# Kernel tuning notes

Hardware: AMD Instinct MI355X
Metric: run time of the kernel (lower is better)

Reference implementation:

```python
import jax, jax.numpy as jnp
import numpy as np

D = 256          # num_channels
H = 4            # num_heads
DH = D // H      # head dim
BN_EPS = 1e-5


def conv1x1(x, W, b):
    # x: [B, Cin, N], W: [Cout, Cin], b: [Cout] -> [B, Cout, N]
    return jnp.einsum('oc,bcn->bon', W, x) + b[None, :, None]


def bn_eval(x, gamma, beta):
    # eval-mode BatchNorm1d with running_mean=0, running_var=1
    scale = gamma / jnp.sqrt(1.0 + BN_EPS)
    return x * scale[None, :, None] + beta[None, :, None]


def setup_inputs() -> dict:
    key = jax.random.key(0)
    ks = jax.random.split(key, 16)
    B, N = 1, 4096
    s = 0.05
    inp = {
        'corr_feat_belief': jax.random.normal(ks[0], (B, D, N), dtype=jnp.float32),
        'spatial_compatibility': jax.random.uniform(ks[1], (B, N, N), dtype=jnp.float32),
        'Wq': jax.random.normal(ks[2], (D, D), dtype=jnp.float32) * s,
        'bq': jnp.zeros((D,), jnp.float32),
        'Wk': jax.random.normal(ks[3], (D, D), dtype=jnp.float32) * s,
        'bk': jnp.zeros((D,), jnp.float32),
        'Wv': jax.random.normal(ks[4], (D, D), dtype=jnp.float32) * s,
        'bv': jnp.zeros((D,), jnp.float32),
        'W1': jax.random.normal(ks[5], (D // 2, D), dtype=jnp.float32) * s,
        'b1': jnp.zeros((D // 2,), jnp.float32),
        'g1': jnp.ones((D // 2,), jnp.float32),
        'be1': jnp.zeros((D // 2,), jnp.float32),
        'W2': jax.random.normal(ks[6], (D // 2, D // 2), dtype=jnp.float32) * s,
        'b2': jnp.zeros((D // 2,), jnp.float32),
        'g2': jnp.ones((D // 2,), jnp.float32),
        'be2': jnp.zeros((D // 2,), jnp.float32),
        'W3': jax.random.normal(ks[7], (D, D // 2), dtype=jnp.float32) * s,
        'b3': jnp.zeros((D,), jnp.float32),
    }
    return inp


def reference(corr_feat_belief, spatial_compatibility, Wq, bq, Wk, bk, Wv, bv,
              W1, b1, g1, be1, W2, b2, g2, be2, W3, b3):
    x = corr_feat_belief                      # [B, D, N]
    B, _, N = x.shape
    # QKV conv1x1 projections, split heads -> [B, H, DH, N]
    Q = conv1x1(x, Wq, bq).reshape(B, H, DH, N)
    K = conv1x1(x, Wk, bk).reshape(B, H, DH, N)
    V = conv1x1(x, Wv, bv).reshape(B, H, DH, N)
    # attention scores [B, H, N, N], scaled
    att = jnp.einsum('bhco,bhci->bhoi', Q, K) / np.sqrt(DH).astype(np.float32)
    # multiplicative spatial-compatibility mask, softmax over keys
    weight = jax.nn.softmax(spatial_compatibility[:, None, :, :] * att, axis=-1)
    message = jnp.einsum('bhoi,bhci->bhco', weight, V).reshape(B, D, N)
    # message MLP: conv1x1 -> BN -> ReLU -> conv1x1 -> BN -> ReLU -> conv1x1
    h = jax.nn.relu(bn_eval(conv1x1(message, W1, b1), g1, be1))
    h = jax.nn.relu(bn_eval(conv1x1(h, W2, b2), g2, be2))
    h = conv1x1(h, W3, b3)
    return x + h
```

## Files before the change

kernel.cpp:

```cpp
#include <hip/hip_runtime.h>
#include <hip/hip_bf16.h>
#include <math.h>

#define D_CH   256
#define NHEAD  4
#define DHEAD  64
#define NPTS   4096
#define KSPLIT 8
#define KCHUNK (NPTS / KSPLIT)
#define BN_RSQ 0.99999500003749963f
#define HSTRIDE 262144

typedef __attribute__((ext_vector_type(4))) float f32x4;
typedef __attribute__((ext_vector_type(8))) short bf16x8;
typedef unsigned short ushort_t;

__device__ __forceinline__ ushort_t f2bf(float x) {
    unsigned int b = __float_as_uint(x);
    return (ushort_t)((b + 0x7FFF + ((b >> 16) & 1)) >> 16);
}
__device__ __forceinline__ float bf2f(ushort_t u) {
    return __uint_as_float(((unsigned int)u) << 16);
}
__device__ __forceinline__ unsigned cvt_pk(float lo, float hi) {
    unsigned r;
    asm("v_cvt_pk_bf16_f32 %0, %1, %2" : "=v"(r) : "v"(lo), "v"(hi));
    return r;
}

__global__ __launch_bounds__(256) void transpose_cast(
    const float* __restrict__ x, ushort_t* __restrict__ xT)
{
    __shared__ float xs[64][65];
    const int tid = threadIdx.x;
    const int n0 = blockIdx.x * 64, k0 = blockIdx.y * 64;
#pragma unroll
    for (int p = 0; p < 16; ++p) {
        int kk = p * 4 + (tid >> 6), nn = tid & 63;
        xs[kk][nn] = x[(size_t)(k0 + kk) * NPTS + n0 + nn];
    }
    __syncthreads();
#pragma unroll
    for (int p = 0; p < 16; ++p) {
        int nn = p * 4 + (tid >> 6), kk = tid & 63;
        xT[(size_t)(n0 + nn) * D_CH + k0 + kk] = f2bf(xs[kk][nn]);
    }
}

__device__ __forceinline__ void gemm_tile_body(
    const float* __restrict__ A, const ushort_t* __restrict__ Bt,
    int K, int m0, int n0, int l15, int lhi, f32x4 acc[2][2])
{
#pragma unroll
    for (int i = 0; i < 2; ++i)
#pragma unroll
        for (int j = 0; j < 2; ++j) acc[i][j] = (f32x4){0.f, 0.f, 0.f, 0.f};

    for (int k0 = 0; k0 < K; k0 += 32) {
        bf16x8 af[2], bfr[2];
#pragma unroll
        for (int mf = 0; mf < 2; ++mf) {
            const float* ap = A + (size_t)(m0 + mf * 16 + l15) * K + k0 + lhi * 8;
            float4 a0 = *(const float4*)ap;
            float4 a1 = *(const float4*)(ap + 4);
            unsigned* tp = (unsigned*)&af[mf];
            tp[0] = cvt_pk(a0.x, a0.y);
            tp[1] = cvt_pk(a0.z, a0.w);
            tp[2] = cvt_pk(a1.x, a1.y);
            tp[3] = cvt_pk(a1.z, a1.w);
        }
#pragma unroll
        for (int nf = 0; nf < 2; ++nf)
            bfr[nf] = *(const bf16x8*)&Bt[(size_t)(n0 + nf * 16 + l15) * K + k0 + lhi * 8];
#pragma unroll
        for (int mf = 0; mf < 2; ++mf)
#pragma unroll
            for (int nf = 0; nf < 2; ++nf)
                acc[mf][nf] = __builtin_amdgcn_mfma_f32_16x16x32_bf16(af[mf], bfr[nf], acc[mf][nf], 0, 0, 0);
    }
}

__global__ __launch_bounds__(256) void gemm_qkv(
    const float* __restrict__ Wq, const float* __restrict__ bq,
    const float* __restrict__ Wk, const float* __restrict__ bk,
    const float* __restrict__ Wv, const float* __restrict__ bv,
    const ushort_t* __restrict__ xT,
    ushort_t* __restrict__ Qf, ushort_t* __restrict__ Kf, ushort_t* __restrict__ Vf)
{
    const int tid = threadIdx.x;
    const int w = tid >> 6, lane = tid & 63, l15 = lane & 15, lhi = lane >> 4;
    const int wm = w >> 1, wn = w & 1;
    const int m0 = blockIdx.y * 64 + wm * 32;
    const int n0 = blockIdx.x * 64 + wn * 32;
    const int z = blockIdx.z;

    const float* A    = (z == 0) ? Wq : (z == 1) ? Wk : Wv;
    const float* bias = (z == 0) ? bq : (z == 1) ? bk : bv;
    ushort_t* dst     = (z == 0) ? Qf : (z == 1) ? Kf : Vf;
    const float scl   = (z == 0) ? 0.125f : 1.0f;

    f32x4 acc[2][2];
    gemm_tile_body(A, xT, D_CH, m0, n0, l15, lhi, acc);

#pragma unroll
    for (int mf = 0; mf < 2; ++mf) {
#pragma unroll
        for (int r = 0; r < 4; ++r) {
            int m = m0 + mf * 16 + lhi * 4 + r;
            int head = m >> 6, dch = m & 63;
            float bi = bias[m];
#pragma unroll
            for (int nf = 0; nf < 2; ++nf) {
                int n = n0 + nf * 16 + l15;
                float v = (acc[mf][nf][r] + bi) * scl;
                size_t idx;
                if (z < 2)
                    idx = (size_t)head * HSTRIDE + (size_t)(n >> 4) * 1024 + (dch >> 5) * 512
                        + (((dch >> 3) & 3) * 16 + (n & 15)) * 8 + (dch & 7);
                else
                    idx = (size_t)head * HSTRIDE + (size_t)(n >> 6) * 4096 + (dch >> 4) * 1024
                        + ((n >> 5) & 1) * 512 + (((n >> 3) & 3) * 16 + (dch & 15)) * 8 + (n & 7);
                dst[idx] = (ushort_t)(cvt_pk(v, v) & 0xFFFF);
            }
        }
    }
}

__device__ __forceinline__ void attn_tile(
    int kt, int ktn, const float* __restrict__ Sg,
    const ushort_t* __restrict__ Kh, const ushort_t* __restrict__ Vh,
    const bf16x8 (&qf)[2][2],
    ushort_t (* __restrict__ Sw)[72],
    f32x4 (&macc)[2][4], float (&lrun)[2],
    ushort_t (* __restrict__ Pw)[72], int l15, int lhi, int lane)
{
    f32x4 sr[8];
#pragma unroll
    for (int p = 0; p < 8; ++p)
        sr[p] = *(const f32x4*)&Sg[(size_t)p * 4 * NPTS + (size_t)ktn * 64];

    bf16x8 vf[8];
    const ushort_t* vb = Vh + (size_t)kt * 4096 + lane * 8;
#pragma unroll
    for (int mm = 0; mm < 2; ++mm)
#pragma unroll
        for (int db = 0; db < 4; ++db)
            vf[mm * 4 + db] = *(const bf16x8*)(vb + db * 1024 + mm * 512);

    f32x4 sacc0[4], sacc1[4];
    __builtin_amdgcn_s_setprio(1);
#pragma unroll
    for (int kb = 0; kb < 4; ++kb) {
        const ushort_t* kp = Kh + (size_t)(kt * 4 + kb) * 1024 + lane * 8;
        bf16x8 kf0 = *(const bf16x8*)kp;
        bf16x8 kf1 = *(const bf16x8*)(kp + 512);
        f32x4 z0 = (f32x4){0.f, 0.f, 0.f, 0.f};
        z0 = __builtin_amdgcn_mfma_f32_16x16x32_bf16(kf0, qf[0][0], z0, 0, 0, 0);
        z0 = __builtin_amdgcn_mfma_f32_16x16x32_bf16(kf1, qf[0][1], z0, 0, 0, 0);
        sacc0[kb] = z0;
        f32x4 z1 = (f32x4){0.f, 0.f, 0.f, 0.f};
        z1 = __builtin_amdgcn_mfma_f32_16x16x32_bf16(kf0, qf[1][0], z1, 0, 0, 0);
        z1 = __builtin_amdgcn_mfma_f32_16x16x32_bf16(kf1, qf[1][1], z1, 0, 0, 0);
        sacc1[kb] = z1;
    }
    __builtin_amdgcn_s_setprio(0);

    float ts0 = 0.0f, ts1 = 0.0f;
#pragma unroll
    for (int kb = 0; kb < 4; ++kb) {
        unsigned a0 = *(const unsigned*)&Sw[l15][kb * 16 + lhi * 4];
        unsigned a1 = *(const unsigned*)&Sw[l15][kb * 16 + lhi * 4 + 2];
        unsigned b0 = *(const unsigned*)&Sw[16 + l15][kb * 16 + lhi * 4];
        unsigned b1 = *(const unsigned*)&Sw[16 + l15][kb * 16 + lhi * 4 + 2];
        float p00 = __expf(sacc0[kb][0] * bf2f((ushort_t)(a0 & 0xFFFF)));
        float p01 = __expf(sacc0[kb][1] * bf2f((ushort_t)(a0 >> 16)));
        float p02 = __expf(sacc0[kb][2] * bf2f((ushort_t)(a1 & 0xFFFF)));
        float p03 = __expf(sacc0[kb][3] * bf2f((ushort_t)(a1 >> 16)));
        float p10 = __expf(sacc1[kb][0] * bf2f((ushort_t)(b0 & 0xFFFF)));
        float p11 = __expf(sacc1[kb][1] * bf2f((ushort_t)(b0 >> 16)));
        float p12 = __expf(sacc1[kb][2] * bf2f((ushort_t)(b1 & 0xFFFF)));
        float p13 = __expf(sacc1[kb][3] * bf2f((ushort_t)(b1 >> 16)));
        ts0 += (p00 + p01) + (p02 + p03);
        ts1 += (p10 + p11) + (p12 + p13);
        *(unsigned*)&Pw[l15][kb * 16 + lhi * 4]          = cvt_pk(p00, p01);
        *(unsigned*)&Pw[l15][kb * 16 + lhi * 4 + 2]      = cvt_pk(p02, p03);
        *(unsigned*)&Pw[16 + l15][kb * 16 + lhi * 4]     = cvt_pk(p10, p11);
        *(unsigned*)&Pw[16 + l15][kb * 16 + lhi * 4 + 2] = cvt_pk(p12, p13);
    }
    lrun[0] += ts0;
    lrun[1] += ts1;

    __builtin_amdgcn_s_setprio(1);
#pragma unroll
    for (int mm = 0; mm < 2; ++mm) {
        bf16x8 pf0 = *(const bf16x8*)&Pw[l15][mm * 32 + lhi * 8];
        bf16x8 pf1 = *(const bf16x8*)&Pw[16 + l15][mm * 32 + lhi * 8];
#pragma unroll
        for (int db = 0; db < 4; ++db) {
            macc[0][db] = __builtin_amdgcn_mfma_f32_16x16x32_bf16(vf[mm * 4 + db], pf0, macc[0][db], 0, 0, 0);
            macc[1][db] = __builtin_amdgcn_mfma_f32_16x16x32_bf16(vf[mm * 4 + db], pf1, macc[1][db], 0, 0, 0);
        }
    }
    __builtin_amdgcn_s_setprio(0);

#pragma unroll
    for (int p = 0; p < 8; ++p) {
        *(unsigned*)&Sw[p * 4 + lhi][l15 * 4]     = cvt_pk(sr[p][0], sr[p][1]);
        *(unsigned*)&Sw[p * 4 + lhi][l15 * 4 + 2] = cvt_pk(sr[p][2], sr[p][3]);
    }
}

__global__ __launch_bounds__(256, 3) void attn_mfma(
    const ushort_t* __restrict__ Qf, const ushort_t* __restrict__ Kf,
    const ushort_t* __restrict__ Vf, const float* __restrict__ S,
    ushort_t* __restrict__ pacc, float* __restrict__ pl)
{
    __shared__ __align__(16) ushort_t P_lds[4][32][72];
    __shared__ __align__(16) ushort_t S_lds[4][32][72];

    const int tid  = threadIdx.x;
    const int w    = tid >> 6;
    const int lane = tid & 63;
    const int l15  = lane & 15;
    const int lhi  = lane >> 4;
    const int h    = blockIdx.y;
    const int ks   = blockIdx.z;
    const int q0   = blockIdx.x * 128 + w * 32;
    const int ktb  = ks * (KCHUNK / 64);

    const ushort_t* Kh = Kf + (size_t)h * HSTRIDE;
    const ushort_t* Vh = Vf + (size_t)h * HSTRIDE;
    const float* Sg = S + (size_t)(q0 + lhi) * NPTS + l15 * 4;
    ushort_t (* __restrict__ Pw)[72] = P_lds[w];
    ushort_t (* __restrict__ Sw)[72] = S_lds[w];

    bf16x8 qf[2][2];
#pragma unroll
    for (int f = 0; f < 2; ++f) {
        const ushort_t* qp = Qf + (size_t)h * HSTRIDE
                           + (size_t)((q0 + f * 16) >> 4) * 1024 + lane * 8;
        qf[f][0] = *(const bf16x8*)qp;
        qf[f][1] = *(const bf16x8*)(qp + 512);
    }

    f32x4 macc[2][4];
#pragma unroll
    for (int f = 0; f < 2; ++f)
#pragma unroll
        for (int db = 0; db < 4; ++db) macc[f][db] = (f32x4){0.f, 0.f, 0.f, 0.f};
    float lrun[2] = {0.0f, 0.0f};

    {
#pragma unroll
        for (int p = 0; p < 8; ++p) {
            f32x4 t = *(const f32x4*)&Sg[(size_t)p * 4 * NPTS + (size_t)ktb * 64];
            *(unsigned*)&Sw[p * 4 + lhi][l15 * 4]     = cvt_pk(t[0], t[1]);
            *(unsigned*)&Sw[p * 4 + lhi][l15 * 4 + 2] = cvt_pk(t[2], t[3]);
        }
    }

    for (int kt = ktb; kt < ktb + 8; ++kt) {
        const int ktn = (kt + 1 < ktb + 8) ? kt + 1 : ktb;
        attn_tile(kt, ktn, Sg, Kh, Vh, qf, Sw, macc, lrun, Pw, l15, lhi, lane);
    }

#pragma unroll
    for (int f = 0; f < 2; ++f) {
        lrun[f] += __shfl_xor(lrun[f], 16);
        lrun[f] += __shfl_xor(lrun[f], 32);
    }

    const size_t pb = ((size_t)ks * NHEAD + h) * NPTS;
#pragma unroll
    for (int f = 0; f < 2; ++f) {
        ushort_t* prow = pacc + (pb + q0 + f * 16 + l15) * DHEAD;
#pragma unroll
        for (int db = 0; db < 4; ++db) {
            *(unsigned*)&prow[db * 16 + lhi * 4]     = cvt_pk(macc[f][db][0], macc[f][db][1]);
            *(unsigned*)&prow[db * 16 + lhi * 4 + 2] = cvt_pk(macc[f][db][2], macc[f][db][3]);
        }
    }
    if (lane < 16) {
        pl[pb + q0 + lane]      = lrun[0];
        pl[pb + q0 + 16 + lane] = lrun[1];
    }
}

__global__ __launch_bounds__(256) void mlp_fused(
    const ushort_t* __restrict__ pacc, const float* __restrict__ pl,
    ushort_t* __restrict__ msgT,
    const float* __restrict__ W1, const float* __restrict__ b1,
    const float* __restrict__ g1, const float* __restrict__ be1,
    const float* __restrict__ W2, const float* __restrict__ b2,
    const float* __restrict__ g2, const float* __restrict__ be2,
    const float* __restrict__ W3, const float* __restrict__ b3,
    const float* __restrict__ x, float* __restrict__ out,
    ushort_t* __restrict__ h1T, ushort_t* __restrict__ h2T)
{
    const int tid = threadIdx.x;
    const int w = tid >> 6, lane = tid & 63, l15 = lane & 15, lhi = lane >> 4;
    const int nblk = blockIdx.x * 16;

    {
        const int hb  = (tid >> 7) * 2;
        const int loc = tid & 127;
        const int ql  = loc >> 3;
        const int d0  = (loc & 7) * 8;
#pragma unroll
        for (int hh = 0; hh < 2; ++hh) {
            const int h = hb + hh;
            float ls = 0.0f;
#pragma unroll
            for (int ks = 0; ks < KSPLIT; ++ks)
                ls += pl[((size_t)ks * NHEAD + h) * NPTS + nblk + ql];
            float inv = 1.0f / ls;
            float o[8];
#pragma unroll
            for (int j = 0; j < 8; ++j) o[j] = 0.0f;
#pragma unroll
            for (int ks = 0; ks < KSPLIT; ++ks) {
                const ushort_t* ap = pacc
                    + (((size_t)ks * NHEAD + h) * NPTS + nblk + ql) * DHEAD + d0;
                bf16x8 v = *(const bf16x8*)ap;
#pragma unroll
                for (int j = 0; j < 8; ++j) o[j] += bf2f((ushort_t)v[j]);
            }
            unsigned* dp = (unsigned*)(msgT + (size_t)(nblk + ql) * D_CH + h * 64 + d0);
            dp[0] = cvt_pk(o[0] * inv, o[1] * inv);
            dp[1] = cvt_pk(o[2] * inv, o[3] * inv);
            dp[2] = cvt_pk(o[4] * inv, o[5] * inv);
            dp[3] = cvt_pk(o[6] * inv, o[7] * inv);
        }
    }
    __syncthreads();

    {
        f32x4 acc[2];
        acc[0] = (f32x4){0.f, 0.f, 0.f, 0.f};
        acc[1] = (f32x4){0.f, 0.f, 0.f, 0.f};
        const ushort_t* Bt = msgT + (size_t)nblk * D_CH;
        for (int k0 = 0; k0 < 256; k0 += 32) {
            bf16x8 bfr = *(const bf16x8*)&Bt[(size_t)l15 * D_CH + k0 + lhi * 8];
#pragma unroll
            for (int mf = 0; mf < 2; ++mf) {
                const float* ap = W1 + (size_t)(w * 32 + mf * 16 + l15) * 256 + k0 + lhi * 8;
                float4 a0 = *(const float4*)ap;
                float4 a1 = *(const float4*)(ap + 4);
                bf16x8 af;
                unsigned* tp = (unsigned*)&af;
                tp[0] = cvt_pk(a0.x, a0.y); tp[1] = cvt_pk(a0.z, a0.w);
                tp[2] = cvt_pk(a1.x, a1.y); tp[3] = cvt_pk(a1.z, a1.w);
                acc[mf] = __builtin_amdgcn_mfma_f32_16x16x32_bf16(af, bfr, acc[mf], 0, 0, 0);
            }
        }
#pragma unroll
        for (int mf = 0; mf < 2; ++mf)
#pragma unroll
            for (int r = 0; r < 4; ++r) {
                int m = w * 32 + mf * 16 + lhi * 4 + r;
                float bi = b1[m], sc = g1[m] * BN_RSQ, sh = be1[m];
                float v = fmaxf((acc[mf][r] + bi) * sc + sh, 0.0f);
                h1T[(size_t)(nblk + l15) * 128 + m] = (ushort_t)(cvt_pk(v, v) & 0xFFFF);
            }
    }
    __syncthreads();

    {
        f32x4 acc[2];
        acc[0] = (f32x4){0.f, 0.f, 0.f, 0.f};
        acc[1] = (f32x4){0.f, 0.f, 0.f, 0.f};
        const ushort_t* Bt = h1T + (size_t)nblk * 128;
        for (int k0 = 0; k0 < 128; k0 += 32) {
            bf16x8 bfr = *(const bf16x8*)&Bt[(size_t)l15 * 128 + k0 + lhi * 8];
#pragma unroll
            for (int mf = 0; mf < 2; ++mf) {
                const float* ap = W2 + (size_t)(w * 32 + mf * 16 + l15) * 128 + k0 + lhi * 8;
                float4 a0 = *(const float4*)ap;
                float4 a1 = *(const float4*)(ap + 4);
                bf16x8 af;
                unsigned* tp = (unsigned*)&af;
                tp[0] = cvt_pk(a0.x, a0.y); tp[1] = cvt_pk(a0.z, a0.w);
                tp[2] = cvt_pk(a1.x, a1.y); tp[3] = cvt_pk(a1.z, a1.w);
                acc[mf] = __builtin_amdgcn_mfma_f32_16x16x32_bf16(af, bfr, acc[mf], 0, 0, 0);
            }
        }
#pragma unroll
        for (int mf = 0; mf < 2; ++mf)
#pragma unroll
            for (int r = 0; r < 4; ++r) {
                int m = w * 32 + mf * 16 + lhi * 4 + r;
                float bi = b2[m], sc = g2[m] * BN_RSQ, sh = be2[m];
                float v = fmaxf((acc[mf][r] + bi) * sc + sh, 0.0f);
                h2T[(size_t)(nblk + l15) * 128 + m] = (ushort_t)(cvt_pk(v, v) & 0xFFFF);
            }
    }
    __syncthreads();

    {
        f32x4 acc[4];
#pragma unroll
        for (int i = 0; i < 4; ++i) acc[i] = (f32x4){0.f, 0.f, 0.f, 0.f};
        const ushort_t* Bt = h2T + (size_t)nblk * 128;
        for (int k0 = 0; k0 < 128; k0 += 32) {
            bf16x8 bfr = *(const bf16x8*)&Bt[(size_t)l15 * 128 + k0 + lhi * 8];
#pragma unroll
            for (int mf = 0; mf < 4; ++mf) {
                const float* ap = W3 + (size_t)(w * 64 + mf * 16 + l15) * 128 + k0 + lhi * 8;
                float4 a0 = *(const float4*)ap;
                float4 a1 = *(const float4*)(ap + 4);
                bf16x8 af;
                unsigned* tp = (unsigned*)&af;
                tp[0] = cvt_pk(a0.x, a0.y); tp[1] = cvt_pk(a0.z, a0.w);
                tp[2] = cvt_pk(a1.x, a1.y); tp[3] = cvt_pk(a1.z, a1.w);
                acc[mf] = __builtin_amdgcn_mfma_f32_16x16x32_bf16(af, bfr, acc[mf], 0, 0, 0);
            }
        }
#pragma unroll
        for (int mf = 0; mf < 4; ++mf)
#pragma unroll
            for (int r = 0; r < 4; ++r) {
                int m = w * 64 + mf * 16 + lhi * 4 + r;
                float bi = b3[m];
                int n = nblk + l15;
                out[(size_t)m * NPTS + n] = acc[mf][r] + bi + x[(size_t)m * NPTS + n];
            }
    }
}

extern "C" void kernel_launch(void* const* d_in, const int* in_sizes, int n_in,
                              void* d_out, int out_size, void* d_ws, size_t ws_size,
                              hipStream_t stream) {
    const float* x  = (const float*)d_in[0];
    const float* S  = (const float*)d_in[1];
    const float* Wq = (const float*)d_in[2];
    const float* bq = (const float*)d_in[3];
    const float* Wk = (const float*)d_in[4];
    const float* bk = (const float*)d_in[5];
    const float* Wv = (const float*)d_in[6];
    const float* bv = (const float*)d_in[7];
    const float* W1 = (const float*)d_in[8];
    const float* b1 = (const float*)d_in[9];
    const float* g1 = (const float*)d_in[10];
    const float* be1= (const float*)d_in[11];
    const float* W2 = (const float*)d_in[12];
    const float* b2 = (const float*)d_in[13];
    const float* g2 = (const float*)d_in[14];
    const float* be2= (const float*)d_in[15];
    const float* W3 = (const float*)d_in[16];
    const float* b3 = (const float*)d_in[17];

    char* ws = (char*)d_ws;
    const size_t MB = 1024 * 1024;
    ushort_t* xT   = (ushort_t*)(ws);
    ushort_t* Qf   = (ushort_t*)(ws + 2 * MB);
    ushort_t* Kf   = (ushort_t*)(ws + 4 * MB);
    ushort_t* Vf   = (ushort_t*)(ws + 6 * MB);
    ushort_t* pacc = (ushort_t*)(ws + 8 * MB);
    float*    pl   = (float*)   (ws + 24 * MB);
    ushort_t* msgT = (ushort_t*)(ws + 25 * MB);
    ushort_t* h1T  = (ushort_t*)(ws + 27 * MB);
    ushort_t* h2T  = (ushort_t*)(ws + 28 * MB);

    transpose_cast<<<dim3(64, 4), 256, 0, stream>>>(x, xT);
    gemm_qkv<<<dim3(64, 4, 3), 256, 0, stream>>>(Wq, bq, Wk, bk, Wv, bv, xT, Qf, Kf, Vf);

    attn_mfma<<<dim3(32, NHEAD, KSPLIT), 256, 0, stream>>>(Qf, Kf, Vf, S, pacc, pl);

    mlp_fused<<<dim3(256), 256, 0, stream>>>(pacc, pl, msgT,
        W1, b1, g1, be1, W2, b2, g2, be2, W3, b3, x, (float*)d_out, h1T, h2T);
}
```

Baseline: 97.79 us.

## Fuse transpose-cast into QKV GEMM and reorder attention tile loads and S stores

Removes the separate transpose_cast kernel: each QKV GEMM block now loads its 64-column slice of x, converts it to bf16, and transposes it into shared memory before the MFMA loop. This drops one launch and the xT global round trip, but every (y,z) block redundantly reloads and converts the same x slice (12x redundant reads). In the attention tile, the V fragment loads move after the QK MFMAs and the next S tile's LDS store moves before the PV MFMAs, to reshape register pressure and overlap.

```diff
diff --git a/kernel.cpp b/kernel.cpp
--- a/kernel.cpp
+++ b/kernel.cpp
@@ -28,39 +28,49 @@
     return r;
 }
 
-__global__ __launch_bounds__(256) void transpose_cast(
-    const float* __restrict__ x, ushort_t* __restrict__ xT)
+__global__ __launch_bounds__(256) void gemm_qkv(
+    const float* __restrict__ Wq, const float* __restrict__ bq,
+    const float* __restrict__ Wk, const float* __restrict__ bk,
+    const float* __restrict__ Wv, const float* __restrict__ bv,
+    const float* __restrict__ x,
+    ushort_t* __restrict__ Qf, ushort_t* __restrict__ Kf, ushort_t* __restrict__ Vf)
 {
-    __shared__ float xs[64][65];
+    __shared__ __align__(16) ushort_t Bs[64][266];
+
     const int tid = threadIdx.x;
-    const int n0 = blockIdx.x * 64, k0 = blockIdx.y * 64;
-#pragma unroll
-    for (int p = 0; p < 16; ++p) {
-        int kk = p * 4 + (tid >> 6), nn = tid & 63;
-        xs[kk][nn] = x[(size_t)(k0 + kk) * NPTS + n0 + nn];
+    const int w = tid >> 6, lane = tid & 63, l15 = lane & 15, lhi = lane >> 4;
+    const int wm = w >> 1, wn = w & 1;
+    const int m0 = blockIdx.y * 64 + wm * 32;
+    const int nb = blockIdx.x * 64;
+    const int z = blockIdx.z;
+
+#pragma unroll
+    for (int kc = 0; kc < 256; kc += 64) {
+#pragma unroll
+        for (int p = 0; p < 16; ++p) {
+            int idx = p * 256 + tid;
+            int kk = idx >> 6, nn = idx & 63;
+            Bs[nn][kc + kk] = f2bf(x[(size_t)(kc + kk) * NPTS + nb + nn]);
+        }
     }
     __syncthreads();
-#pragma unroll
-    for (int p = 0; p < 16; ++p) {
-        int nn = p * 4 + (tid >> 6), kk = tid & 63;
-        xT[(size_t)(n0 + nn) * D_CH + k0 + kk] = f2bf(xs[kk][nn]);
-    }
-}
-
-__device__ __forceinline__ void gemm_tile_body(
-    const float* __restrict__ A, const ushort_t* __restrict__ Bt,
-    int K, int m0, int n0, int l15, int lhi, f32x4 acc[2][2])
-{
+
+    const float* A    = (z == 0) ? Wq : (z == 1) ? Wk : Wv;
+    const float* bias = (z == 0) ? bq : (z == 1) ? bk : bv;
+    ushort_t* dst     = (z == 0) ? Qf : (z == 1) ? Kf : Vf;
+    const float scl   = (z == 0) ? 0.125f : 1.0f;
+
+    f32x4 acc[2][2];
 #pragma unroll
     for (int i = 0; i < 2; ++i)
 #pragma unroll
         for (int j = 0; j < 2; ++j) acc[i][j] = (f32x4){0.f, 0.f, 0.f, 0.f};
 
-    for (int k0 = 0; k0 < K; k0 += 32) {
+    for (int k0 = 0; k0 < D_CH; k0 += 32) {
         bf16x8 af[2], bfr[2];
 #pragma unroll
         for (int mf = 0; mf < 2; ++mf) {
-            const float* ap = A + (size_t)(m0 + mf * 16 + l15) * K + k0 + lhi * 8;
+            const float* ap = A + (size_t)(m0 + mf * 16 + l15) * D_CH + k0 + lhi * 8;
             float4 a0 = *(const float4*)ap;
             float4 a1 = *(const float4*)(ap + 4);
             unsigned* tp = (unsigned*)&af[mf];
@@ -71,36 +81,13 @@
         }
 #pragma unroll
         for (int nf = 0; nf < 2; ++nf)
-            bfr[nf] = *(const bf16x8*)&Bt[(size_t)(n0 + nf * 16 + l15) * K + k0 + lhi * 8];
+            bfr[nf] = *(const bf16x8*)&Bs[wn * 32 + nf * 16 + l15][k0 + lhi * 8];
 #pragma unroll
         for (int mf = 0; mf < 2; ++mf)
 #pragma unroll
             for (int nf = 0; nf < 2; ++nf)
                 acc[mf][nf] = __builtin_amdgcn_mfma_f32_16x16x32_bf16(af[mf], bfr[nf], acc[mf][nf], 0, 0, 0);
     }
-}
-
-__global__ __launch_bounds__(256) void gemm_qkv(
-    const float* __restrict__ Wq, const float* __restrict__ bq,
-    const float* __restrict__ Wk, const float* __restrict__ bk,
-    const float* __restrict__ Wv, const float* __restrict__ bv,
-    const ushort_t* __restrict__ xT,
-    ushort_t* __restrict__ Qf, ushort_t* __restrict__ Kf, ushort_t* __restrict__ Vf)
-{
-    const int tid = threadIdx.x;
-    const int w = tid >> 6, lane = tid & 63, l15 = lane & 15, lhi = lane >> 4;
-    const int wm = w >> 1, wn = w & 1;
-    const int m0 = blockIdx.y * 64 + wm * 32;
-    const int n0 = blockIdx.x * 64 + wn * 32;
-    const int z = blockIdx.z;
-
-    const float* A    = (z == 0) ? Wq : (z == 1) ? Wk : Wv;
-    const float* bias = (z == 0) ? bq : (z == 1) ? bk : bv;
-    ushort_t* dst     = (z == 0) ? Qf : (z == 1) ? Kf : Vf;
-    const float scl   = (z == 0) ? 0.125f : 1.0f;
-
-    f32x4 acc[2][2];
-    gemm_tile_body(A, xT, D_CH, m0, n0, l15, lhi, acc);
 
 #pragma unroll
     for (int mf = 0; mf < 2; ++mf) {
@@ -111,7 +98,7 @@
             float bi = bias[m];
 #pragma unroll
             for (int nf = 0; nf < 2; ++nf) {
-                int n = n0 + nf * 16 + l15;
+                int n = nb + wn * 32 + nf * 16 + l15;
                 float v = (acc[mf][nf][r] + bi) * scl;
                 size_t idx;
                 if (z < 2)
@@ -138,14 +125,6 @@
 #pragma unroll
     for (int p = 0; p < 8; ++p)
         sr[p] = *(const f32x4*)&Sg[(size_t)p * 4 * NPTS + (size_t)ktn * 64];
-
-    bf16x8 vf[8];
-    const ushort_t* vb = Vh + (size_t)kt * 4096 + lane * 8;
-#pragma unroll
-    for (int mm = 0; mm < 2; ++mm)
-#pragma unroll
-        for (int db = 0; db < 4; ++db)
-            vf[mm * 4 + db] = *(const bf16x8*)(vb + db * 1024 + mm * 512);
 
     f32x4 sacc0[4], sacc1[4];
     __builtin_amdgcn_s_setprio(1);
@@ -164,6 +143,14 @@
         sacc1[kb] = z1;
     }
     __builtin_amdgcn_s_setprio(0);
+
+    bf16x8 vf[8];
+    const ushort_t* vb = Vh + (size_t)kt * 4096 + lane * 8;
+#pragma unroll
+    for (int mm = 0; mm < 2; ++mm)
+#pragma unroll
+        for (int db = 0; db < 4; ++db)
+            vf[mm * 4 + db] = *(const bf16x8*)(vb + db * 1024 + mm * 512);
 
     float ts0 = 0.0f, ts1 = 0.0f;
 #pragma unroll
@@ -190,6 +177,12 @@
     lrun[0] += ts0;
     lrun[1] += ts1;
 
+#pragma unroll
+    for (int p = 0; p < 8; ++p) {
+        *(unsigned*)&Sw[p * 4 + lhi][l15 * 4]     = cvt_pk(sr[p][0], sr[p][1]);
+        *(unsigned*)&Sw[p * 4 + lhi][l15 * 4 + 2] = cvt_pk(sr[p][2], sr[p][3]);
+    }
+
     __builtin_amdgcn_s_setprio(1);
 #pragma unroll
     for (int mm = 0; mm < 2; ++mm) {
@@ -202,12 +195,6 @@
         }
     }
     __builtin_amdgcn_s_setprio(0);
-
-#pragma unroll
-    for (int p = 0; p < 8; ++p) {
-        *(unsigned*)&Sw[p * 4 + lhi][l15 * 4]     = cvt_pk(sr[p][0], sr[p][1]);
-        *(unsigned*)&Sw[p * 4 + lhi][l15 * 4 + 2] = cvt_pk(sr[p][2], sr[p][3]);
-    }
 }
 
 __global__ __launch_bounds__(256, 3) void attn_mfma(
@@ -451,7 +438,6 @@
 
     char* ws = (char*)d_ws;
     const size_t MB = 1024 * 1024;
-    ushort_t* xT   = (ushort_t*)(ws);
     ushort_t* Qf   = (ushort_t*)(ws + 2 * MB);
     ushort_t* Kf   = (ushort_t*)(ws + 4 * MB);
     ushort_t* Vf   = (ushort_t*)(ws + 6 * MB);
@@ -461,8 +447,7 @@
     ushort_t* h1T  = (ushort_t*)(ws + 27 * MB);
     ushort_t* h2T  = (ushort_t*)(ws + 28 * MB);
 
-    transpose_cast<<<dim3(64, 4), 256, 0, stream>>>(x, xT);
-    gemm_qkv<<<dim3(64, 4, 3), 256, 0, stream>>>(Wq, bq, Wk, bk, Wv, bv, xT, Qf, Kf, Vf);
+    gemm_qkv<<<dim3(64, 4, 3), 256, 0, stream>>>(Wq, bq, Wk, bk, Wv, bv, x, Qf, Kf, Vf);
 
     attn_mfma<<<dim3(32, NHEAD, KSPLIT), 256, 0, stream>>>(Qf, Kf, Vf, S, pacc, pl);
 
```

Measured after the change: 85.72 us (median of 2 runs). 12.3% less time.
